# Optimization experiments

Hardware: AMD Instinct MI355X
Metric: run time of the kernel (lower is better)

The kernel has to match this reference:

```python
import jax, jax.numpy as jnp
import numpy as np

N = 8192
PERCENT_ON = 0.1
K = int(round(N * PERCENT_ON))  # 819
BOOST_STRENGTH = 1.0


def setup_inputs() -> dict:
    key = jax.random.key(0)
    k1, k2 = jax.random.split(key)
    x = jax.random.normal(k1, (4096, N), dtype=jnp.float32)
    duty_cycles = jax.random.uniform(k2, (N,), dtype=jnp.float32) * 0.2
    return {"x": x, "duty_cycles": duty_cycles}


def reference(x, duty_cycles):
    # boost factors: exp((target_density - duty_cycle) * boost_strength)
    boost_strength = jnp.maximum(jnp.float32(BOOST_STRENGTH), 0.0)
    target_density = jnp.float32(K / N)
    boost_factors = jnp.exp((target_density - duty_cycles) * boost_strength)
    boosted = x * boost_factors  # [B, N]
    # top-k on boosted values, but transmit ORIGINAL x values at winning units
    _, idx = jax.lax.top_k(boosted, K)  # idx: [B, K]
    updates = jnp.take_along_axis(x, idx, axis=1)  # [B, K]
    rows = jnp.arange(x.shape[0])[:, None]  # [B, 1]
    out = jnp.zeros_like(x).at[rows, idx].set(updates)
    return out
```

## Files before the change

### kernel.cpp

```cpp
#include <hip/hip_runtime.h>
#include <math.h>

#define NCOL 8192
#define NROW 4096
#define KSEL 819
#define TPB  256
#define VPT  8
#define HSTRIDE 2048

__device__ __align__(16) float g_boost[NCOL];

__global__ void boost_kernel(const float* __restrict__ duty) {
    int i = blockIdx.x * blockDim.x + threadIdx.x;
    if (i < NCOL) {
        float diff = (0.0999755859375f - duty[i]);
        g_boost[i] = (float)exp((double)diff);
    }
}

__device__ __forceinline__ unsigned f2k(float f) {
    unsigned u = __float_as_uint(f);
    return u ^ (0x80000000u | (unsigned)((int)u >> 31));
}

__global__ __launch_bounds__(TPB) void kwinners_kernel(const float* __restrict__ x,
                                                       float* __restrict__ out) {
    __shared__ __align__(16) unsigned char smem[16384];
    __shared__ int lds_wtot[4];
    __shared__ int lds_selarr[3], lds_Rarr[3];
    __shared__ int lds_E, lds_cnt;

    int* hist = (int*)smem;

    const int t = threadIdx.x;
    const int row = blockIdx.x;
    const int lane = t & 63;
    const int w = t >> 6;

    const float4* x4 = (const float4*)(x + (size_t)row * NCOL);
    const float4* b4 = (const float4*)g_boost;

    unsigned kr[VPT][4];

    {
        const int4 z = make_int4(0, 0, 0, 0);
        int4* h4 = (int4*)hist;
        h4[4 * t + 0] = z; h4[4 * t + 1] = z; h4[4 * t + 2] = z; h4[4 * t + 3] = z;
    }

#pragma unroll
    for (int j = 0; j < VPT; ++j) {
        const int v = t + TPB * j;
        float4 xx = x4[v];
        float4 bb = b4[v];
        kr[j][0] = f2k(xx.x * bb.x);
        kr[j][1] = f2k(xx.y * bb.y);
        kr[j][2] = f2k(xx.z * bb.z);
        kr[j][3] = f2k(xx.w * bb.w);
    }
    __syncthreads();

    unsigned prefix = 0;
#pragma unroll
    for (int p = 0; p < 3; ++p) {
        const int sh  = (p == 0) ? 21 : (p == 1) ? 10 : 0;
        const int nb  = (p == 2) ? 1024 : 2048;
        const int bpt = nb / TPB;
        int* myh = hist + ((lane >= 32) ? HSTRIDE : 0);

        if (p == 0) {
#pragma unroll
            for (int j = 0; j < VPT; ++j)
#pragma unroll
                for (int c = 0; c < 4; ++c)
                    atomicAdd(&myh[kr[j][c] >> 21], 1);
        } else {
            const int shp = (p == 1) ? 21 : 10;
#pragma unroll
            for (int j = 0; j < VPT; ++j)
#pragma unroll
                for (int c = 0; c < 4; ++c) {
                    const unsigned key = kr[j][c];
                    if ((key >> shp) == (prefix >> shp))
                        atomicAdd(&myh[(key >> sh) & (nb - 1)], 1);
                }
        }
        __syncthreads();

        int arr[8];
        int ts = 0;
        {
            const int i4 = t * (bpt >> 2);
            int4* h4a = (int4*)hist;
            int4* h4b = (int4*)(hist + HSTRIDE);
            const int4 z = make_int4(0, 0, 0, 0);
            int4 a0 = h4a[i4], b0 = h4b[i4];
            arr[0] = a0.x + b0.x; arr[1] = a0.y + b0.y;
            arr[2] = a0.z + b0.z; arr[3] = a0.w + b0.w;
            h4a[i4] = z; h4b[i4] = z;
            if (bpt == 8) {
                int4 a1 = h4a[i4 + 1], b1 = h4b[i4 + 1];
                arr[4] = a1.x + b1.x; arr[5] = a1.y + b1.y;
                arr[6] = a1.z + b1.z; arr[7] = a1.w + b1.w;
                h4a[i4 + 1] = z; h4b[i4 + 1] = z;
            }
#pragma unroll
            for (int b = 0; b < 8; ++b) if (b < bpt) ts += arr[b];
        }
        int s = ts;
#pragma unroll
        for (int off = 1; off < 64; off <<= 1) {
            int o = __shfl_down(s, off);
            if (lane + off < 64) s += o;
        }
        if (lane == 0) lds_wtot[w] = s;
        __syncthreads();

        int S_later = 0;
#pragma unroll
        for (int w2 = 0; w2 < 4; ++w2) if (w2 > w) S_later += lds_wtot[w2];
        const int S_above = (s - ts) + S_later;
        const int R0 = (p == 0) ? KSEL : lds_Rarr[p - 1];
        if (S_above < R0 && S_above + ts >= R0) {
            int cum = S_above;
            int selb = 0, selR = 0, selE = 0;
#pragma unroll
            for (int b = 7; b >= 0; --b) {
                if (b < bpt) {
                    const int nx = cum + arr[b];
                    if (cum < R0 && nx >= R0) { selb = t * bpt + b; selR = R0 - cum; selE = arr[b]; }
                    cum = nx;
                }
            }
            lds_selarr[p] = selb;
            lds_Rarr[p] = selR;
            if (p == 2) lds_E = selE;
        }
        __syncthreads();
        prefix |= ((unsigned)lds_selarr[p]) << sh;
    }

    const unsigned thresh = prefix;
    const int Rf = lds_Rarr[2];
    const int E = lds_E;
    unsigned dropm = 0;

    if (E > Rf) {
        unsigned short* list = (unsigned short*)smem;
        if (t == 0) lds_cnt = 0;
        __syncthreads();
#pragma unroll
        for (int j = 0; j < VPT; ++j)
#pragma unroll
            for (int c = 0; c < 4; ++c) {
                if (kr[j][c] == thresh) {
                    int slot = atomicAdd(&lds_cnt, 1);
                    list[slot] = (unsigned short)(4 * (t + TPB * j) + c);
                }
            }
        __syncthreads();
        const int n = lds_cnt;
#pragma unroll
        for (int j = 0; j < VPT; ++j)
#pragma unroll
            for (int c = 0; c < 4; ++c) {
                if (kr[j][c] == thresh) {
                    const int col = 4 * (t + TPB * j) + c;
                    int rank = 0;
                    for (int i = 0; i < n; ++i) rank += (list[i] < col) ? 1 : 0;
                    if (rank >= Rf) dropm |= (1u << (4 * j + c));
                }
            }
    }

    float4* o4 = (float4*)(out + (size_t)row * NCOL);
#pragma unroll
    for (int j = 0; j < VPT; ++j) {
        const int v = t + TPB * j;
        float4 xx = x4[v];
        float4 r;
        r.x = (kr[j][0] >= thresh && !((dropm >> (4 * j + 0)) & 1u)) ? xx.x : 0.0f;
        r.y = (kr[j][1] >= thresh && !((dropm >> (4 * j + 1)) & 1u)) ? xx.y : 0.0f;
        r.z = (kr[j][2] >= thresh && !((dropm >> (4 * j + 2)) & 1u)) ? xx.z : 0.0f;
        r.w = (kr[j][3] >= thresh && !((dropm >> (4 * j + 3)) & 1u)) ? xx.w : 0.0f;
        o4[v] = r;
    }
}

extern "C" void kernel_launch(void* const* d_in, const int* in_sizes, int n_in,
                              void* d_out, int out_size, void* d_ws, size_t ws_size,
                              hipStream_t stream) {
    const float* x = (const float*)d_in[0];
    const float* duty = (const float*)d_in[1];
    float* out = (float*)d_out;
    (void)in_sizes; (void)n_in; (void)out_size; (void)d_ws; (void)ws_size;

    boost_kernel<<<(NCOL + TPB - 1) / TPB, TPB, 0, stream>>>(duty);
    kwinners_kernel<<<NROW, TPB, 0, stream>>>(x, out);
}
```

Baseline: 71.86 us.

## Replace three-pass radix select with pivot-bucketed single histogram and exact fallback

Replaces the three-pass radix histogram select with one pass that histograms only keys above a fixed pivot (chosen from the expected distribution) into 2048 buckets. The winning bucket's keys go into a small LDS list, and the exact threshold is found by pairwise ranking. A slower 4-pass 8-bit radix select runs as a fallback when the pivot or list capacity assumptions fail. It also uses nontemporal stores for the output. The aim is fewer histogram passes and fewer LDS atomics and barriers per row, at the cost of relying on the input distribution for the fast path.

```diff
diff --git a/kernel.cpp b/kernel.cpp
--- a/kernel.cpp
+++ b/kernel.cpp
@@ -6,7 +6,11 @@
 #define KSEL 819
 #define TPB  256
 #define VPT  8
-#define HSTRIDE 2048
+#define LCAP 256
+#define KPIV 0xBF866666u
+#define NBKT 2048
+
+typedef float f32x4 __attribute__((ext_vector_type(4)));
 
 __device__ __align__(16) float g_boost[NCOL];
 
@@ -23,36 +27,38 @@
     return u ^ (0x80000000u | (unsigned)((int)u >> 31));
 }
 
+__device__ __forceinline__ int kbucket(unsigned k) {
+    int b = (int)(k >> 13) - (int)(KPIV >> 13);
+    return (b > NBKT - 1) ? (NBKT - 1) : b;
+}
+
 __global__ __launch_bounds__(TPB) void kwinners_kernel(const float* __restrict__ x,
                                                        float* __restrict__ out) {
     __shared__ __align__(16) unsigned char smem[16384];
     __shared__ int lds_wtot[4];
-    __shared__ int lds_selarr[3], lds_Rarr[3];
-    __shared__ int lds_E, lds_cnt;
+    __shared__ int lds_C, lds_cnt, lds_sel, lds_R1, lds_fE, lds_fR;
+    __shared__ unsigned lds_th;
 
     int* hist = (int*)smem;
-
-    const int t = threadIdx.x;
-    const int row = blockIdx.x;
-    const int lane = t & 63;
-    const int w = t >> 6;
-
-    const float4* x4 = (const float4*)(x + (size_t)row * NCOL);
-    const float4* b4 = (const float4*)g_boost;
+    unsigned* lkey = (unsigned*)(smem + 8192);
+
+    const int t = threadIdx.x, row = blockIdx.x, lane = t & 63, w = t >> 6;
+    const f32x4* x4 = (const f32x4*)(x + (size_t)row * NCOL);
+    const f32x4* b4 = (const f32x4*)g_boost;
 
     unsigned kr[VPT][4];
 
     {
+        int4* h4 = (int4*)hist;
         const int4 z = make_int4(0, 0, 0, 0);
-        int4* h4 = (int4*)hist;
-        h4[4 * t + 0] = z; h4[4 * t + 1] = z; h4[4 * t + 2] = z; h4[4 * t + 3] = z;
+        h4[2 * t] = z; h4[2 * t + 1] = z;
+        if (t == 0) { lds_C = 0; lds_cnt = 0; lds_th = 0xFFFFFFFFu; }
     }
 
 #pragma unroll
     for (int j = 0; j < VPT; ++j) {
-        const int v = t + TPB * j;
-        float4 xx = x4[v];
-        float4 bb = b4[v];
+        f32x4 xx = x4[t + TPB * j];
+        f32x4 bb = b4[t + TPB * j];
         kr[j][0] = f2k(xx.x * bb.x);
         kr[j][1] = f2k(xx.y * bb.y);
         kr[j][2] = f2k(xx.z * bb.z);
@@ -60,53 +66,31 @@
     }
     __syncthreads();
 
-    unsigned prefix = 0;
-#pragma unroll
-    for (int p = 0; p < 3; ++p) {
-        const int sh  = (p == 0) ? 21 : (p == 1) ? 10 : 0;
-        const int nb  = (p == 2) ? 1024 : 2048;
-        const int bpt = nb / TPB;
-        int* myh = hist + ((lane >= 32) ? HSTRIDE : 0);
-
-        if (p == 0) {
-#pragma unroll
-            for (int j = 0; j < VPT; ++j)
-#pragma unroll
-                for (int c = 0; c < 4; ++c)
-                    atomicAdd(&myh[kr[j][c] >> 21], 1);
-        } else {
-            const int shp = (p == 1) ? 21 : 10;
-#pragma unroll
-            for (int j = 0; j < VPT; ++j)
-#pragma unroll
-                for (int c = 0; c < 4; ++c) {
-                    const unsigned key = kr[j][c];
-                    if ((key >> shp) == (prefix >> shp))
-                        atomicAdd(&myh[(key >> sh) & (nb - 1)], 1);
-                }
-        }
-        __syncthreads();
-
+    int cnt = 0;
+#pragma unroll
+    for (int j = 0; j < VPT; ++j)
+#pragma unroll
+        for (int c = 0; c < 4; ++c) {
+            unsigned k = kr[j][c];
+            if (k > KPIV) { ++cnt; atomicAdd(&hist[kbucket(k)], 1); }
+        }
+#pragma unroll
+    for (int off = 32; off; off >>= 1) cnt += __shfl_down(cnt, off);
+    if (lane == 0) atomicAdd(&lds_C, cnt);
+    __syncthreads();
+    const int C = lds_C;
+
+    unsigned th = 0; int Rf = 0, E = 0; bool ok = false;
+
+    if (C >= KSEL) {
         int arr[8];
-        int ts = 0;
         {
-            const int i4 = t * (bpt >> 2);
-            int4* h4a = (int4*)hist;
-            int4* h4b = (int4*)(hist + HSTRIDE);
-            const int4 z = make_int4(0, 0, 0, 0);
-            int4 a0 = h4a[i4], b0 = h4b[i4];
-            arr[0] = a0.x + b0.x; arr[1] = a0.y + b0.y;
-            arr[2] = a0.z + b0.z; arr[3] = a0.w + b0.w;
-            h4a[i4] = z; h4b[i4] = z;
-            if (bpt == 8) {
-                int4 a1 = h4a[i4 + 1], b1 = h4b[i4 + 1];
-                arr[4] = a1.x + b1.x; arr[5] = a1.y + b1.y;
-                arr[6] = a1.z + b1.z; arr[7] = a1.w + b1.w;
-                h4a[i4 + 1] = z; h4b[i4 + 1] = z;
-            }
-#pragma unroll
-            for (int b = 0; b < 8; ++b) if (b < bpt) ts += arr[b];
-        }
+            int4 a0 = ((const int4*)hist)[2 * t];
+            int4 a1 = ((const int4*)hist)[2 * t + 1];
+            arr[0] = a0.x; arr[1] = a0.y; arr[2] = a0.z; arr[3] = a0.w;
+            arr[4] = a1.x; arr[5] = a1.y; arr[6] = a1.z; arr[7] = a1.w;
+        }
+        int ts = arr[0] + arr[1] + arr[2] + arr[3] + arr[4] + arr[5] + arr[6] + arr[7];
         int s = ts;
 #pragma unroll
         for (int off = 1; off < 64; off <<= 1) {
@@ -115,75 +99,139 @@
         }
         if (lane == 0) lds_wtot[w] = s;
         __syncthreads();
-
         int S_later = 0;
 #pragma unroll
         for (int w2 = 0; w2 < 4; ++w2) if (w2 > w) S_later += lds_wtot[w2];
-        const int S_above = (s - ts) + S_later;
-        const int R0 = (p == 0) ? KSEL : lds_Rarr[p - 1];
-        if (S_above < R0 && S_above + ts >= R0) {
-            int cum = S_above;
-            int selb = 0, selR = 0, selE = 0;
+        const int S_ab = (s - ts) + S_later;
+        if (S_ab < KSEL && S_ab + ts >= KSEL) {
+            int cum = S_ab, selb = 0, r1 = 0;
 #pragma unroll
             for (int b = 7; b >= 0; --b) {
-                if (b < bpt) {
-                    const int nx = cum + arr[b];
-                    if (cum < R0 && nx >= R0) { selb = t * bpt + b; selR = R0 - cum; selE = arr[b]; }
-                    cum = nx;
-                }
-            }
-            lds_selarr[p] = selb;
-            lds_Rarr[p] = selR;
-            if (p == 2) lds_E = selE;
-        }
-        __syncthreads();
-        prefix |= ((unsigned)lds_selarr[p]) << sh;
-    }
-
-    const unsigned thresh = prefix;
-    const int Rf = lds_Rarr[2];
-    const int E = lds_E;
+                int nx = cum + arr[b];
+                if (cum < KSEL && nx >= KSEL) { selb = 8 * t + b; r1 = KSEL - cum; }
+                cum = nx;
+            }
+            lds_sel = selb; lds_R1 = r1;
+        }
+        __syncthreads();
+        const int sel = lds_sel, R1 = lds_R1;
+
+#pragma unroll
+        for (int j = 0; j < VPT; ++j)
+#pragma unroll
+            for (int c = 0; c < 4; ++c) {
+                unsigned k = kr[j][c];
+                if (kbucket(k) == sel) {
+                    int sl = atomicAdd(&lds_cnt, 1);
+                    if (sl < LCAP) lkey[sl] = k;
+                }
+            }
+        __syncthreads();
+        const int n = lds_cnt;
+        if (n <= LCAP) {
+            if (t < n) {
+                unsigned myk = lkey[t];
+                int g = 0, e = 0;
+                for (int i = 0; i < n; ++i) {
+                    unsigned k2 = lkey[i];
+                    g += (k2 > myk) ? 1 : 0;
+                    e += (k2 == myk) ? 1 : 0;
+                }
+                if (g < R1 && g + e >= R1) lds_th = myk;
+            }
+            __syncthreads();
+            th = lds_th;
+            int ge = 0;
+#pragma unroll
+            for (int j = 0; j < VPT; ++j)
+#pragma unroll
+                for (int c = 0; c < 4; ++c) {
+                    unsigned k = kr[j][c];
+                    ge += (k > th ? 1 : 0) + (k == th ? (1 << 16) : 0);
+                }
+#pragma unroll
+            for (int off = 32; off; off >>= 1) ge += __shfl_down(ge, off);
+            if (lane == 0) lds_wtot[w] = ge;
+            __syncthreads();
+            const int GE = lds_wtot[0] + lds_wtot[1] + lds_wtot[2] + lds_wtot[3];
+            const int G = GE & 0xFFFF, Eg = GE >> 16;
+            if (G < KSEL && G + Eg >= KSEL) { ok = true; Rf = KSEL - G; E = Eg; }
+        }
+    }
+
+    if (!ok) {
+        unsigned prefix = 0; int R = KSEL;
+        for (int p = 0; p < 4; ++p) {
+            const int sh = 24 - 8 * p;
+            hist[t] = 0;
+            __syncthreads();
+#pragma unroll
+            for (int j = 0; j < VPT; ++j)
+#pragma unroll
+                for (int c = 0; c < 4; ++c) {
+                    unsigned k = kr[j][c];
+                    if (p == 0 || (k >> (sh + 8)) == (prefix >> (sh + 8)))
+                        atomicAdd(&hist[(k >> sh) & 255u], 1);
+                }
+            __syncthreads();
+            int h = hist[t], s2 = h;
+#pragma unroll
+            for (int off = 1; off < 64; off <<= 1) {
+                int o = __shfl_down(s2, off);
+                if (lane + off < 64) s2 += o;
+            }
+            if (lane == 0) lds_wtot[w] = s2;
+            __syncthreads();
+            int S_later = 0;
+#pragma unroll
+            for (int w2 = 0; w2 < 4; ++w2) if (w2 > w) S_later += lds_wtot[w2];
+            const int S_ab = (s2 - h) + S_later;
+            if (S_ab < R && S_ab + h >= R) { lds_sel = t; lds_fR = R - S_ab; lds_fE = h; }
+            __syncthreads();
+            prefix |= ((unsigned)lds_sel) << sh;
+            R = lds_fR;
+        }
+        th = prefix; Rf = R; E = lds_fE;
+    }
+
     unsigned dropm = 0;
-
     if (E > Rf) {
-        unsigned short* list = (unsigned short*)smem;
+        unsigned short* tl = (unsigned short*)smem;
+        __syncthreads();
         if (t == 0) lds_cnt = 0;
         __syncthreads();
 #pragma unroll
         for (int j = 0; j < VPT; ++j)
 #pragma unroll
-            for (int c = 0; c < 4; ++c) {
-                if (kr[j][c] == thresh) {
-                    int slot = atomicAdd(&lds_cnt, 1);
-                    list[slot] = (unsigned short)(4 * (t + TPB * j) + c);
-                }
-            }
-        __syncthreads();
-        const int n = lds_cnt;
+            for (int c = 0; c < 4; ++c)
+                if (kr[j][c] == th) {
+                    int sl = atomicAdd(&lds_cnt, 1);
+                    tl[sl] = (unsigned short)(4 * (t + TPB * j) + c);
+                }
+        __syncthreads();
+        const int ntie = lds_cnt;
 #pragma unroll
         for (int j = 0; j < VPT; ++j)
 #pragma unroll
-            for (int c = 0; c < 4; ++c) {
-                if (kr[j][c] == thresh) {
+            for (int c = 0; c < 4; ++c)
+                if (kr[j][c] == th) {
                     const int col = 4 * (t + TPB * j) + c;
                     int rank = 0;
-                    for (int i = 0; i < n; ++i) rank += (list[i] < col) ? 1 : 0;
+                    for (int i = 0; i < ntie; ++i) rank += (tl[i] < col) ? 1 : 0;
                     if (rank >= Rf) dropm |= (1u << (4 * j + c));
                 }
-            }
-    }
-
-    float4* o4 = (float4*)(out + (size_t)row * NCOL);
+    }
+
+    f32x4* o4 = (f32x4*)(out + (size_t)row * NCOL);
 #pragma unroll
     for (int j = 0; j < VPT; ++j) {
-        const int v = t + TPB * j;
-        float4 xx = x4[v];
-        float4 r;
-        r.x = (kr[j][0] >= thresh && !((dropm >> (4 * j + 0)) & 1u)) ? xx.x : 0.0f;
-        r.y = (kr[j][1] >= thresh && !((dropm >> (4 * j + 1)) & 1u)) ? xx.y : 0.0f;
-        r.z = (kr[j][2] >= thresh && !((dropm >> (4 * j + 2)) & 1u)) ? xx.z : 0.0f;
-        r.w = (kr[j][3] >= thresh && !((dropm >> (4 * j + 3)) & 1u)) ? xx.w : 0.0f;
-        o4[v] = r;
+        f32x4 xx = x4[t + TPB * j];
+        f32x4 r;
+        r.x = (kr[j][0] >= th && !((dropm >> (4 * j + 0)) & 1u)) ? xx.x : 0.0f;
+        r.y = (kr[j][1] >= th && !((dropm >> (4 * j + 1)) & 1u)) ? xx.y : 0.0f;
+        r.z = (kr[j][2] >= th && !((dropm >> (4 * j + 2)) & 1u)) ? xx.z : 0.0f;
+        r.w = (kr[j][3] >= th && !((dropm >> (4 * j + 3)) & 1u)) ? xx.w : 0.0f;
+        __builtin_nontemporal_store(r, &o4[t + TPB * j]);
     }
 }
 
```

Result: faster. 63.76 us (-11.3%).
